# Kernel tuning notes

Measured on AMD Instinct MI355X. Metric: run time of the kernel, lower is better.

The kernel has to match this reference:

```python
import jax, jax.numpy as jnp
import numpy as np

TEMPERATURE = 0.1
EPS = 1e-12  # matches torch F.normalize eps


def setup_inputs() -> dict:
    key = jax.random.key(0)
    k1, k2 = jax.random.split(key)
    B, T, C = 8, 1024, 512
    x = jax.random.normal(k1, (B, T, C), dtype=jnp.float32)
    quantized = jax.random.normal(k2, (B, T, C), dtype=jnp.float32)
    return {"x": x, "quantized": quantized}


def reference(x, quantized):
    B, T, C = x.shape
    xf = x.reshape(-1, C)            # (N, C)
    qf = quantized.reshape(-1, C)    # (N, C)
    xn = xf / jnp.maximum(jnp.linalg.norm(xf, axis=-1, keepdims=True), EPS)
    qn = qf / jnp.maximum(jnp.linalg.norm(qf, axis=-1, keepdims=True), EPS)
    # (N, N) similarity logits
    sim = jnp.matmul(xn, qn.T) / TEMPERATURE
    N = sim.shape[0]
    # cross-entropy with targets = arange(N): loss_i = logsumexp(sim_i) - sim_ii
    logZ = jax.nn.logsumexp(sim, axis=-1)
    diag = jnp.diagonal(sim)
    loss = jnp.mean(logZ - diag)
    predictions = jnp.argmax(sim, axis=-1)
    targets = jnp.arange(N)
    accuracy = jnp.mean((predictions == targets).astype(jnp.float32))
    return loss, accuracy
```

## Files before the change

kernel.cpp:

```cpp
#include <hip/hip_runtime.h>
#include <hip/hip_bf16.h>
#include <math.h>

#define CDIM 512
#define NROW 8192
#define BM 256
#define BN 256
#define BK 32
#define NT 16
#define NCB 32
#define BUFSZ 32768
#define TEMP_INV 10.0f

typedef unsigned short u16;
typedef u16  u16x8 __attribute__((ext_vector_type(8)));
typedef __bf16 bf16x8 __attribute__((ext_vector_type(8)));
typedef float  f32x4 __attribute__((ext_vector_type(4)));

static __device__ __forceinline__ float bf2f(u16 u) {
    return __uint_as_float(((unsigned)u) << 16);
}
static __device__ __forceinline__ u16 f2bf(float f) {
    unsigned u = __float_as_uint(f);
    return (u16)((u + 0x7FFFu + ((u >> 16) & 1u)) >> 16);
}

static __device__ __forceinline__ void gload_lds16(const u16* g, char* l) {
    __builtin_amdgcn_global_load_lds(
        (const __attribute__((address_space(1))) void*)g,
        (__attribute__((address_space(3))) void*)l, 16, 0, 0);
}

__global__ __launch_bounds__(256) void norm_split_kernel(
    const float* __restrict__ x, const float* __restrict__ q,
    u16* __restrict__ xh, u16* __restrict__ qh, int n)
{
    int wave = blockIdx.x * 4 + (threadIdx.x >> 6);
    int lane = threadIdx.x & 63;
    const float* src; u16* dh; int row;
    if (wave < n) { src = x; dh = xh; row = wave; }
    else          { src = q; dh = qh; row = wave - n; }

    const float4* p = reinterpret_cast<const float4*>(src + (size_t)row * CDIM);
    float4 a = p[lane * 2];
    float4 b = p[lane * 2 + 1];
    float v[8] = {a.x, a.y, a.z, a.w, b.x, b.y, b.z, b.w};
    float ss = 0.f;
#pragma unroll
    for (int j = 0; j < 8; ++j) ss += v[j] * v[j];
#pragma unroll
    for (int off = 32; off; off >>= 1) ss += __shfl_xor(ss, off);
    float scale = 1.0f / fmaxf(sqrtf(ss), 1e-12f);

    u16 h[8] __attribute__((aligned(16)));
#pragma unroll
    for (int j = 0; j < 8; ++j) h[j] = f2bf(v[j] * scale);
    *(u16x8*)&dh[(size_t)row * CDIM + lane * 8] = *(u16x8*)h;
}

__global__ __launch_bounds__(1024, 4) void sim_main_kernel(
    const u16* __restrict__ xh, const u16* __restrict__ qh,
    float4* __restrict__ part)
{
    extern __shared__ __align__(16) char smem[];
    const int t = threadIdx.x, lane = t & 63, wid = t >> 6;
    const int wm = wid >> 2, wn = wid & 3;

    const int orig = blockIdx.x;
    const int xcd = orig & 7, s = orig >> 3;
    const int rb = s >> 2;
    const int cb = xcd * 4 + (s & 3);
    const int row0 = rb * BM, col0 = cb * BN;

    const int schunk = (t & 3) ^ ((t >> 3) & 3);
    const u16* sa = xh + (size_t)(row0 + (t >> 2)) * CDIM + schunk * 8;
    const u16* sb = qh + (size_t)(col0 + (t >> 2)) * CDIM + schunk * 8;
    const unsigned dstw = (unsigned)wid * 1024u;

    auto stage = [&](int kt) {
        char* b = smem + (kt % 3) * BUFSZ;
        const int ko = kt * BK;
        gload_lds16(sa + ko, b + dstw);
        gload_lds16(sb + ko, b + 16384 + dstw);
    };

    const unsigned kxc = ((unsigned)((lane >> 4) ^ ((lane >> 1) & 3))) * 16u;
    const unsigned aro = ((unsigned)(wm * 64 + (lane & 15))) * 64u + kxc;
    const unsigned bro = 16384u + ((unsigned)(wn * 64 + (lane & 15))) * 64u + kxc;

    f32x4 acc[4][4];
#pragma unroll
    for (int i = 0; i < 4; ++i)
#pragma unroll
        for (int j = 0; j < 4; ++j) acc[i][j] = (f32x4){0.f, 0.f, 0.f, 0.f};

    stage(0); stage(1);
    asm volatile("s_waitcnt vmcnt(2)" ::: "memory");
    __builtin_amdgcn_s_barrier();
    asm volatile("" ::: "memory");

    for (int kt = 0; kt < NT; ++kt) {
        const char* buf = smem + (kt % 3) * BUFSZ;
        if (kt < NT - 2) stage(kt + 2);
        bf16x8 afr[4], bfr[4];
#pragma unroll
        for (int mf = 0; mf < 4; ++mf) afr[mf] = *(const bf16x8*)(buf + aro + mf * 1024u);
#pragma unroll
        for (int nf = 0; nf < 4; ++nf) bfr[nf] = *(const bf16x8*)(buf + bro + nf * 1024u);

        __builtin_amdgcn_s_setprio(1);
#pragma unroll
        for (int mf = 0; mf < 4; ++mf)
#pragma unroll
            for (int nf = 0; nf < 4; ++nf)
                acc[mf][nf] = __builtin_amdgcn_mfma_f32_16x16x32_bf16(
                    afr[mf], bfr[nf], acc[mf][nf], 0, 0, 0);
        __builtin_amdgcn_s_setprio(0);

        if (kt < NT - 2)       { asm volatile("s_waitcnt vmcnt(2)" ::: "memory"); }
        else if (kt == NT - 2) { asm volatile("s_waitcnt vmcnt(0)" ::: "memory"); }
        asm volatile("s_waitcnt lgkmcnt(0)" ::: "memory");
        __builtin_amdgcn_s_barrier();
        asm volatile("" ::: "memory");
    }

    __syncthreads();
    float* sm = (float*)smem;
    float* sl = sm + 1024;
    int*   si = (int*)(sl + 1024);
    float* sd = (float*)(si + 1024);
    const int g = lane >> 4;
#pragma unroll
    for (int mf = 0; mf < 4; ++mf) {
#pragma unroll
        for (int r = 0; r < 4; ++r) {
            const int row_loc  = wm * 64 + mf * 16 + g * 4 + r;
            const int row_glob = row0 + row_loc;
            const int ci = col0 + wn * 64 + (lane & 15);
            float vmax = acc[mf][0][r];
            int cbest = ci;
#pragma unroll
            for (int nf = 1; nf < 4; ++nf) {
                float v = acc[mf][nf][r];
                if (v > vmax) { vmax = v; cbest = ci + nf * 16; }
                if (ci + nf * 16 == row_glob) sd[row_loc] = v * TEMP_INV;
            }
            if (ci == row_glob) sd[row_loc] = acc[mf][0][r] * TEMP_INV;
#pragma unroll
            for (int m = 1; m < 16; m <<= 1) {
                float ov = __shfl_xor(vmax, m);
                int   oi = __shfl_xor(cbest, m);
                if (ov > vmax || (ov == vmax && oi < cbest)) { vmax = ov; cbest = oi; }
            }
            float ssum = 0.f;
#pragma unroll
            for (int nf = 0; nf < 4; ++nf)
                ssum += __expf((acc[mf][nf][r] - vmax) * TEMP_INV);
#pragma unroll
            for (int m = 1; m < 16; m <<= 1) ssum += __shfl_xor(ssum, m);
            if ((lane & 15) == 0) {
                sm[row_loc * 4 + wn] = vmax * TEMP_INV;
                sl[row_loc * 4 + wn] = ssum;
                si[row_loc * 4 + wn] = cbest;
            }
        }
    }
    __syncthreads();
    if (t < 256) {
        float M = sm[t * 4];
#pragma unroll
        for (int w = 1; w < 4; ++w) M = fmaxf(M, sm[t * 4 + w]);
        float L = 0.f;
#pragma unroll
        for (int w = 0; w < 4; ++w) L += sl[t * 4 + w] * __expf(sm[t * 4 + w] - M);
        float bv = -1e30f; int bi = 0;
#pragma unroll
        for (int w = 0; w < 4; ++w) {
            float v = sm[t * 4 + w];
            if (v > bv) { bv = v; bi = si[t * 4 + w]; }
        }
        part[(size_t)(row0 + t) * NCB + cb] =
            make_float4(M, L, __int_as_float(bi), sd[t]);
    }
}

__global__ __launch_bounds__(256) void merge_kernel(
    const float4* __restrict__ part,
    float* __restrict__ loss_arr, float* __restrict__ corr_arr)
{
    int i    = blockIdx.x * 4 + (threadIdx.x >> 6);
    int lane = threadIdx.x & 63;
    float4 v = part[(size_t)i * NCB + (lane & 31)];

    float M = v.x;
#pragma unroll
    for (int off = 32; off; off >>= 1) M = fmaxf(M, __shfl_xor(M, off));
    float L = (lane < 32) ? v.y * __expf(v.x - M) : 0.f;
#pragma unroll
    for (int off = 32; off; off >>= 1) L += __shfl_xor(L, off);
    float bm = v.x; int bi = __float_as_int(v.z);
#pragma unroll
    for (int off = 1; off < 32; off <<= 1) {
        float ov = __shfl_xor(bm, off);
        int   oi = __shfl_xor(bi, off);
        if (ov > bm || (ov == bm && oi < bi)) { bm = ov; bi = oi; }
    }
    float dg = __shfl(v.w, i >> 8);
    if (lane == 0) {
        loss_arr[i] = (M + logf(L)) - dg;
        corr_arr[i] = (bi == i) ? 1.0f : 0.0f;
    }
}

__global__ __launch_bounds__(256) void finalize_kernel(
    const float* __restrict__ loss_arr, const float* __restrict__ corr_arr,
    float* __restrict__ out, int n)
{
    float a = 0.f, b = 0.f;
    for (int i = threadIdx.x; i < n; i += 256) { a += loss_arr[i]; b += corr_arr[i]; }
#pragma unroll
    for (int off = 32; off; off >>= 1) { a += __shfl_xor(a, off); b += __shfl_xor(b, off); }
    __shared__ float sa[4], sb[4];
    int wid = threadIdx.x >> 6, lane = threadIdx.x & 63;
    if (lane == 0) { sa[wid] = a; sb[wid] = b; }
    __syncthreads();
    if (threadIdx.x == 0) {
        out[0] = (sa[0] + sa[1] + sa[2] + sa[3]) / n;
        out[1] = (sb[0] + sb[1] + sb[2] + sb[3]) / n;
    }
}

extern "C" void kernel_launch(void* const* d_in, const int* in_sizes, int n_in,
                              void* d_out, int out_size, void* d_ws, size_t ws_size,
                              hipStream_t stream)
{
    const float* x = (const float*)d_in[0];
    const float* q = (const float*)d_in[1];
    const int n = in_sizes[0] / CDIM;

    char* ws = (char*)d_ws;
    size_t sz_bf = (size_t)n * CDIM * sizeof(u16);
    u16* xh = (u16*)(ws);
    u16* qh = (u16*)(ws + sz_bf);
    char* p = ws + 2 * sz_bf;
    float4* part = (float4*)p; p += (size_t)n * NCB * sizeof(float4);
    float* loss_arr = (float*)p; p += (size_t)n * 4;
    float* corr_arr = (float*)p;

    norm_split_kernel<<<(2 * n) / 4, 256, 0, stream>>>(x, q, xh, qh, n);

    sim_main_kernel<<<(n / BM) * (n / BN), 1024, 3 * BUFSZ, stream>>>(xh, qh, part);

    merge_kernel<<<n / 4, 256, 0, stream>>>(part, loss_arr, corr_arr);

    finalize_kernel<<<1, 256, 0, stream>>>(loss_arr, corr_arr, (float*)d_out, n);
}
```

Before: 122.6 us.

## Use 8-wave 128x64 warp tiles with BK=64 double-buffered phased pipeline

The similarity GEMM moves from 16 waves with 64x64 per-wave tiles, BK=32 and a triple buffer to 8 waves with 128x64 per-wave tiles, BK=64 and a 128KB double buffer. Each k-step is split into four phases, and each phase interleaves loading part of the next tile with MFMA work on the current one, using staged vmcnt waits and a new XOR swizzle. The aim is more register-level reuse per LDS read and fewer barriers per unit of work. The cost is fewer waves to hide latency, higher accumulator register pressure and a larger LDS footprint. The epilogue row mapping is updated to the new wave layout.

```diff
diff --git a/kernel.cpp b/kernel.cpp
--- a/kernel.cpp
+++ b/kernel.cpp
@@ -6,10 +6,9 @@
 #define NROW 8192
 #define BM 256
 #define BN 256
-#define BK 32
-#define NT 16
+#define BK 64
+#define NT 8
 #define NCB 32
-#define BUFSZ 32768
 #define TEMP_INV 10.0f
 
 typedef unsigned short u16;
@@ -58,7 +57,7 @@
     *(u16x8*)&dh[(size_t)row * CDIM + lane * 8] = *(u16x8*)h;
 }
 
-__global__ __launch_bounds__(1024, 4) void sim_main_kernel(
+__global__ __launch_bounds__(512, 2) void sim_main_kernel(
     const u16* __restrict__ xh, const u16* __restrict__ qh,
     float4* __restrict__ part)
 {
@@ -72,57 +71,103 @@
     const int cb = xcd * 4 + (s & 3);
     const int row0 = rb * BM, col0 = cb * BN;
 
-    const int schunk = (t & 3) ^ ((t >> 3) & 3);
-    const u16* sa = xh + (size_t)(row0 + (t >> 2)) * CDIM + schunk * 8;
-    const u16* sb = qh + (size_t)(col0 + (t >> 2)) * CDIM + schunk * 8;
-    const unsigned dstw = (unsigned)wid * 1024u;
-
-    auto stage = [&](int kt) {
-        char* b = smem + (kt % 3) * BUFSZ;
-        const int ko = kt * BK;
-        gload_lds16(sa + ko, b + dstw);
-        gload_lds16(sb + ko, b + 16384 + dstw);
-    };
-
-    const unsigned kxc = ((unsigned)((lane >> 4) ^ ((lane >> 1) & 3))) * 16u;
-    const unsigned aro = ((unsigned)(wm * 64 + (lane & 15))) * 64u + kxc;
-    const unsigned bro = 16384u + ((unsigned)(wn * 64 + (lane & 15))) * 64u + kxc;
-
-    f32x4 acc[4][4];
-#pragma unroll
-    for (int i = 0; i < 4; ++i)
+    const int hh = t >> 8;
+    const int rr = (t >> 3) & 31;
+    const int rB = t >> 3;
+    const unsigned blog = (((unsigned)t & 7u) * 16u) ^ ((((unsigned)t >> 3) & 7u) << 4);
+    const u16* sA = xh + (size_t)(row0 + hh * 128 + rr) * CDIM + blog / 2;
+    const u16* sB = qh + (size_t)(col0 + rB) * CDIM + blog / 2;
+
+    const unsigned kx0 = ((((unsigned)lane >> 4)) * 16u) ^ ((((unsigned)lane & 7u)) << 4);
+    const unsigned kx1 = (64u + (((unsigned)lane >> 4)) * 16u) ^ ((((unsigned)lane & 7u)) << 4);
+    const unsigned abase = (unsigned)wm * 4096u + (unsigned)(lane & 15) * 128u;
+    const unsigned bbase = 32768u + (unsigned)wn * 8192u + (unsigned)(lane & 15) * 128u;
+
+    f32x4 acc[8][4];
+#pragma unroll
+    for (int i = 0; i < 8; ++i)
 #pragma unroll
         for (int j = 0; j < 4; ++j) acc[i][j] = (f32x4){0.f, 0.f, 0.f, 0.f};
 
-    stage(0); stage(1);
-    asm volatile("s_waitcnt vmcnt(2)" ::: "memory");
+#define STAGE_A(BUF, KT, C) gload_lds16(sA + (size_t)(C) * (32 * CDIM) + (KT) * BK, \
+        smem + (BUF) * 65536 + (C) * 8192 + wid * 1024)
+#define STAGE_B(BUF, KT, W) gload_lds16(sB + (size_t)(W) * (64 * CDIM) + (KT) * BK, \
+        smem + (BUF) * 65536 + 32768 + (W) * 8192 + wid * 1024)
+
+#define READ_A(P)                                                              \
+    afr[0][0] = *(const bf16x8*)(buf + abase + (P) * 8192u + kx0);             \
+    afr[0][1] = *(const bf16x8*)(buf + abase + (P) * 8192u + kx1);             \
+    afr[1][0] = *(const bf16x8*)(buf + abase + (P) * 8192u + 2048u + kx0);     \
+    afr[1][1] = *(const bf16x8*)(buf + abase + (P) * 8192u + 2048u + kx1);
+
+#define PHASE_MFMA(MF0)                                                        \
+    __builtin_amdgcn_s_setprio(1);                                             \
+    _Pragma("unroll")                                                          \
+    for (int ks = 0; ks < 2; ++ks)                                             \
+        _Pragma("unroll")                                                      \
+        for (int m = 0; m < 2; ++m)                                            \
+            _Pragma("unroll")                                                  \
+            for (int nf = 0; nf < 4; ++nf)                                     \
+                acc[(MF0) + m][nf] = __builtin_amdgcn_mfma_f32_16x16x32_bf16(  \
+                    afr[m][ks], bfr[nf][ks], acc[(MF0) + m][nf], 0, 0, 0);     \
+    __builtin_amdgcn_s_setprio(0);
+
+#define BAR() asm volatile("" ::: "memory"); __builtin_amdgcn_s_barrier(); asm volatile("" ::: "memory")
+
+    STAGE_B(0, 0, 0); STAGE_B(0, 0, 1); STAGE_B(0, 0, 2); STAGE_B(0, 0, 3);
+    STAGE_A(0, 0, 0); STAGE_A(0, 0, 1); STAGE_A(0, 0, 2); STAGE_A(0, 0, 3);
+    asm volatile("s_waitcnt vmcnt(0)" ::: "memory");
     __builtin_amdgcn_s_barrier();
     asm volatile("" ::: "memory");
 
     for (int kt = 0; kt < NT; ++kt) {
-        const char* buf = smem + (kt % 3) * BUFSZ;
-        if (kt < NT - 2) stage(kt + 2);
-        bf16x8 afr[4], bfr[4];
-#pragma unroll
-        for (int mf = 0; mf < 4; ++mf) afr[mf] = *(const bf16x8*)(buf + aro + mf * 1024u);
-#pragma unroll
-        for (int nf = 0; nf < 4; ++nf) bfr[nf] = *(const bf16x8*)(buf + bro + nf * 1024u);
-
-        __builtin_amdgcn_s_setprio(1);
-#pragma unroll
-        for (int mf = 0; mf < 4; ++mf)
-#pragma unroll
-            for (int nf = 0; nf < 4; ++nf)
-                acc[mf][nf] = __builtin_amdgcn_mfma_f32_16x16x32_bf16(
-                    afr[mf], bfr[nf], acc[mf][nf], 0, 0, 0);
-        __builtin_amdgcn_s_setprio(0);
-
-        if (kt < NT - 2)       { asm volatile("s_waitcnt vmcnt(2)" ::: "memory"); }
-        else if (kt == NT - 2) { asm volatile("s_waitcnt vmcnt(0)" ::: "memory"); }
+        const char* buf = smem + (unsigned)(kt & 1) * 65536u;
+        const int nb = (kt + 1) & 1;
+        const bool pf = (kt + 1 < NT);
+        bf16x8 bfr[4][2], afr[2][2];
+
+        asm volatile("s_waitcnt vmcnt(3)" ::: "memory");
+#pragma unroll
+        for (int nf = 0; nf < 4; ++nf) {
+            bfr[nf][0] = *(const bf16x8*)(buf + bbase + nf * 2048u + kx0);
+            bfr[nf][1] = *(const bf16x8*)(buf + bbase + nf * 2048u + kx1);
+        }
+        READ_A(0)
+        if (pf) { STAGE_B(nb, kt + 1, 0); STAGE_B(nb, kt + 1, 1); }
+        BAR();
         asm volatile("s_waitcnt lgkmcnt(0)" ::: "memory");
-        __builtin_amdgcn_s_barrier();
-        asm volatile("" ::: "memory");
-    }
+        PHASE_MFMA(0)
+        BAR();
+
+        asm volatile("s_waitcnt vmcnt(4)" ::: "memory");
+        READ_A(1)
+        if (pf) { STAGE_B(nb, kt + 1, 2); STAGE_B(nb, kt + 1, 3); }
+        BAR();
+        asm volatile("s_waitcnt lgkmcnt(0)" ::: "memory");
+        PHASE_MFMA(2)
+        BAR();
+
+        asm volatile("s_waitcnt vmcnt(5)" ::: "memory");
+        READ_A(2)
+        if (pf) { STAGE_A(nb, kt + 1, 0); STAGE_A(nb, kt + 1, 1); }
+        BAR();
+        asm volatile("s_waitcnt lgkmcnt(0)" ::: "memory");
+        PHASE_MFMA(4)
+        BAR();
+
+        asm volatile("s_waitcnt vmcnt(6)" ::: "memory");
+        READ_A(3)
+        if (pf) { STAGE_A(nb, kt + 1, 2); STAGE_A(nb, kt + 1, 3); }
+        BAR();
+        asm volatile("s_waitcnt lgkmcnt(0)" ::: "memory");
+        PHASE_MFMA(6)
+        BAR();
+    }
+#undef STAGE_A
+#undef STAGE_B
+#undef READ_A
+#undef PHASE_MFMA
+#undef BAR
 
     __syncthreads();
     float* sm = (float*)smem;
@@ -131,10 +176,10 @@
     float* sd = (float*)(si + 1024);
     const int g = lane >> 4;
 #pragma unroll
-    for (int mf = 0; mf < 4; ++mf) {
+    for (int mf = 0; mf < 8; ++mf) {
 #pragma unroll
         for (int r = 0; r < 4; ++r) {
-            const int row_loc  = wm * 64 + mf * 16 + g * 4 + r;
+            const int row_loc  = wm * 128 + mf * 16 + g * 4 + r;
             const int row_glob = row0 + row_loc;
             const int ci = col0 + wn * 64 + (lane & 15);
             float vmax = acc[mf][0][r];
@@ -249,7 +294,7 @@
 
     norm_split_kernel<<<(2 * n) / 4, 256, 0, stream>>>(x, q, xh, qh, n);
 
-    sim_main_kernel<<<(n / BM) * (n / BN), 1024, 3 * BUFSZ, stream>>>(xh, qh, part);
+    sim_main_kernel<<<(n / BM) * (n / BN), 512, 131072, stream>>>(xh, qh, part);
 
     merge_kernel<<<n / 4, 256, 0, stream>>>(part, loss_arr, corr_arr);
 
```

Measured after the change: 156.3 us. 1.27x slower.

## Persistent blocks loop over column tiles, stream B from global, fixed-shift logsumexp

Applied to the files above, without the earlier changes.

The sim kernel now launches 256 blocks of 512 threads. Each block owns a 256-row A tile and loops over four column tiles. A is staged in LDS through a triple buffer, while each warp loads its B fragments straight from global into registers, double-buffered across k-steps, and computes a 128x64 sub-tile. The logsumexp drops the running max and subtracts a fixed constant of 10, which relies on unit-normalized vectors bounding logits by 1/T, so the merge skips its max rescale. This cuts LDS traffic and launch count, but it lowers occupancy, raises register pressure, and makes B reads uncoalesced per lane.

```diff
diff --git a/kernel.cpp b/kernel.cpp
--- a/kernel.cpp
+++ b/kernel.cpp
@@ -7,9 +7,8 @@
 #define BM 256
 #define BN 256
 #define BK 32
-#define NT 16
+#define GTOT 64
 #define NCB 32
-#define BUFSZ 32768
 #define TEMP_INV 10.0f
 
 typedef unsigned short u16;
@@ -58,130 +57,152 @@
     *(u16x8*)&dh[(size_t)row * CDIM + lane * 8] = *(u16x8*)h;
 }
 
-__global__ __launch_bounds__(1024, 4) void sim_main_kernel(
+__global__ __launch_bounds__(512, 2) void sim_main_kernel(
     const u16* __restrict__ xh, const u16* __restrict__ qh,
     float4* __restrict__ part)
 {
     extern __shared__ __align__(16) char smem[];
     const int t = threadIdx.x, lane = t & 63, wid = t >> 6;
     const int wm = wid >> 2, wn = wid & 3;
-
-    const int orig = blockIdx.x;
-    const int xcd = orig & 7, s = orig >> 3;
-    const int rb = s >> 2;
-    const int cb = xcd * 4 + (s & 3);
-    const int row0 = rb * BM, col0 = cb * BN;
+    const int xcd = blockIdx.x & 7, rb = blockIdx.x >> 3;
+    const int row0 = rb * BM;
 
     const int schunk = (t & 3) ^ ((t >> 3) & 3);
-    const u16* sa = xh + (size_t)(row0 + (t >> 2)) * CDIM + schunk * 8;
-    const u16* sb = qh + (size_t)(col0 + (t >> 2)) * CDIM + schunk * 8;
-    const unsigned dstw = (unsigned)wid * 1024u;
-
-    auto stage = [&](int kt) {
-        char* b = smem + (kt % 3) * BUFSZ;
-        const int ko = kt * BK;
-        gload_lds16(sa + ko, b + dstw);
-        gload_lds16(sb + ko, b + 16384 + dstw);
-    };
+    const u16* sa0 = xh + (size_t)(row0 + (t >> 2)) * CDIM + schunk * 8;
+    const u16* sa1 = sa0 + 128 * CDIM;
 
     const unsigned kxc = ((unsigned)((lane >> 4) ^ ((lane >> 1) & 3))) * 16u;
-    const unsigned aro = ((unsigned)(wm * 64 + (lane & 15))) * 64u + kxc;
-    const unsigned bro = 16384u + ((unsigned)(wn * 64 + (lane & 15))) * 64u + kxc;
-
-    f32x4 acc[4][4];
-#pragma unroll
-    for (int i = 0; i < 4; ++i)
-#pragma unroll
-        for (int j = 0; j < 4; ++j) acc[i][j] = (f32x4){0.f, 0.f, 0.f, 0.f};
-
-    stage(0); stage(1);
-    asm volatile("s_waitcnt vmcnt(2)" ::: "memory");
+    const unsigned aro = ((unsigned)(wm * 128 + (lane & 15))) * 64u + kxc;
+
+    const u16* pBl = qh + (size_t)(lane & 15) * CDIM + (lane >> 4) * 8;
+
+#define STAGE_A(G) do {                                                        \
+        char* b_ = smem + ((G) % 3) * 16384;                                   \
+        const int ko_ = ((G) & 15) * BK;                                       \
+        gload_lds16(sa0 + ko_, b_ + wid * 1024);                               \
+        gload_lds16(sa1 + ko_, b_ + 8192 + wid * 1024);                        \
+    } while (0)
+
+#define LOAD_B(DST, GN) do {                                                   \
+        const int col0n_ = (xcd * 4 + ((GN) >> 4)) * BN;                       \
+        const u16* pn_ = pBl + (size_t)(col0n_ + wn * 64) * CDIM               \
+                         + ((GN) & 15) * BK;                                   \
+        _Pragma("unroll")                                                      \
+        for (int nf_ = 0; nf_ < 4; ++nf_)                                      \
+            DST[nf_] = *(const bf16x8*)(pn_ + (size_t)nf_ * 16 * CDIM);        \
+    } while (0)
+
+    f32x4 acc[8][4];
+    bf16x8 Bc[4], Bn[4];
+
+    STAGE_A(0); STAGE_A(1);
+    LOAD_B(Bc, 0);
+    asm volatile("s_waitcnt vmcnt(6)" ::: "memory");
     __builtin_amdgcn_s_barrier();
     asm volatile("" ::: "memory");
 
-    for (int kt = 0; kt < NT; ++kt) {
-        const char* buf = smem + (kt % 3) * BUFSZ;
-        if (kt < NT - 2) stage(kt + 2);
-        bf16x8 afr[4], bfr[4];
-#pragma unroll
-        for (int mf = 0; mf < 4; ++mf) afr[mf] = *(const bf16x8*)(buf + aro + mf * 1024u);
-#pragma unroll
-        for (int nf = 0; nf < 4; ++nf) bfr[nf] = *(const bf16x8*)(buf + bro + nf * 1024u);
-
-        __builtin_amdgcn_s_setprio(1);
-#pragma unroll
-        for (int mf = 0; mf < 4; ++mf)
-#pragma unroll
-            for (int nf = 0; nf < 4; ++nf)
-                acc[mf][nf] = __builtin_amdgcn_mfma_f32_16x16x32_bf16(
-                    afr[mf], bfr[nf], acc[mf][nf], 0, 0, 0);
-        __builtin_amdgcn_s_setprio(0);
-
-        if (kt < NT - 2)       { asm volatile("s_waitcnt vmcnt(2)" ::: "memory"); }
-        else if (kt == NT - 2) { asm volatile("s_waitcnt vmcnt(0)" ::: "memory"); }
-        asm volatile("s_waitcnt lgkmcnt(0)" ::: "memory");
-        __builtin_amdgcn_s_barrier();
-        asm volatile("" ::: "memory");
-    }
-
-    __syncthreads();
-    float* sm = (float*)smem;
-    float* sl = sm + 1024;
-    int*   si = (int*)(sl + 1024);
-    float* sd = (float*)(si + 1024);
-    const int g = lane >> 4;
-#pragma unroll
-    for (int mf = 0; mf < 4; ++mf) {
-#pragma unroll
-        for (int r = 0; r < 4; ++r) {
-            const int row_loc  = wm * 64 + mf * 16 + g * 4 + r;
-            const int row_glob = row0 + row_loc;
-            const int ci = col0 + wn * 64 + (lane & 15);
-            float vmax = acc[mf][0][r];
-            int cbest = ci;
-#pragma unroll
-            for (int nf = 1; nf < 4; ++nf) {
-                float v = acc[mf][nf][r];
-                if (v > vmax) { vmax = v; cbest = ci + nf * 16; }
-                if (ci + nf * 16 == row_glob) sd[row_loc] = v * TEMP_INV;
-            }
-            if (ci == row_glob) sd[row_loc] = acc[mf][0][r] * TEMP_INV;
-#pragma unroll
-            for (int m = 1; m < 16; m <<= 1) {
-                float ov = __shfl_xor(vmax, m);
-                int   oi = __shfl_xor(cbest, m);
-                if (ov > vmax || (ov == vmax && oi < cbest)) { vmax = ov; cbest = oi; }
-            }
-            float ssum = 0.f;
-#pragma unroll
-            for (int nf = 0; nf < 4; ++nf)
-                ssum += __expf((acc[mf][nf][r] - vmax) * TEMP_INV);
-#pragma unroll
-            for (int m = 1; m < 16; m <<= 1) ssum += __shfl_xor(ssum, m);
-            if ((lane & 15) == 0) {
-                sm[row_loc * 4 + wn] = vmax * TEMP_INV;
-                sl[row_loc * 4 + wn] = ssum;
-                si[row_loc * 4 + wn] = cbest;
+#define KT_HALF(KT, CUR, NXT)                                                  \
+    {                                                                          \
+        const int g = c * 16 + (KT);                                           \
+        if ((KT) < 14 || c < 3) STAGE_A(g + 2);                                \
+        if ((KT) < 15 || c < 3) LOAD_B(NXT, g + 1);                            \
+        const char* buf = smem + (g % 3) * 16384;                              \
+        bf16x8 afr[8];                                                         \
+        _Pragma("unroll")                                                      \
+        for (int mf = 0; mf < 8; ++mf)                                         \
+            afr[mf] = *(const bf16x8*)(buf + aro + mf * 1024u);                \
+        if ((KT) == 15 && c == 3) { asm volatile("s_waitcnt vmcnt(0)" ::: "memory"); } \
+        else                      { asm volatile("s_waitcnt vmcnt(6)" ::: "memory"); } \
+        __builtin_amdgcn_s_setprio(1);                                         \
+        _Pragma("unroll")                                                      \
+        for (int mf = 0; mf < 8; ++mf)                                         \
+            _Pragma("unroll")                                                  \
+            for (int nf = 0; nf < 4; ++nf)                                     \
+                acc[mf][nf] = __builtin_amdgcn_mfma_f32_16x16x32_bf16(         \
+                    afr[mf], CUR[nf], acc[mf][nf], 0, 0, 0);                   \
+        __builtin_amdgcn_s_setprio(0);                                         \
+        asm volatile("s_waitcnt lgkmcnt(0)" ::: "memory");                     \
+        __builtin_amdgcn_s_barrier();                                          \
+        asm volatile("" ::: "memory");                                         \
+    }
+
+    for (int c = 0; c < 4; ++c) {
+        const int cb = xcd * 4 + c;
+        const int col0 = cb * BN;
+
+#pragma unroll
+        for (int i = 0; i < 8; ++i)
+#pragma unroll
+            for (int j = 0; j < 4; ++j) acc[i][j] = (f32x4){0.f, 0.f, 0.f, 0.f};
+
+#pragma unroll
+        for (int kt2 = 0; kt2 < 8; ++kt2) {
+            KT_HALF(kt2 * 2,     Bc, Bn)
+            KT_HALF(kt2 * 2 + 1, Bn, Bc)
+        }
+
+        __syncthreads();
+        float* sm = (float*)(smem + 49152);
+        float* sl = sm + 1024;
+        int*   si = (int*)(sl + 1024);
+        float* sd = (float*)(si + 1024);
+        const int g4 = lane >> 4;
+#pragma unroll
+        for (int mf = 0; mf < 8; ++mf) {
+#pragma unroll
+            for (int r = 0; r < 4; ++r) {
+                const int row_loc  = wm * 128 + mf * 16 + g4 * 4 + r;
+                const int row_glob = row0 + row_loc;
+                const int ci = col0 + wn * 64 + (lane & 15);
+                float vmax = acc[mf][0][r];
+                int cbest = ci;
+#pragma unroll
+                for (int nf = 1; nf < 4; ++nf) {
+                    float v = acc[mf][nf][r];
+                    if (v > vmax) { vmax = v; cbest = ci + nf * 16; }
+                    if (ci + nf * 16 == row_glob) sd[row_loc] = v * TEMP_INV;
+                }
+                if (ci == row_glob) sd[row_loc] = acc[mf][0][r] * TEMP_INV;
+#pragma unroll
+                for (int m = 1; m < 16; m <<= 1) {
+                    float ov = __shfl_xor(vmax, m);
+                    int   oi = __shfl_xor(cbest, m);
+                    if (ov > vmax || (ov == vmax && oi < cbest)) { vmax = ov; cbest = oi; }
+                }
+                float ssum = 0.f;
+#pragma unroll
+                for (int nf = 0; nf < 4; ++nf)
+                    ssum += __expf(acc[mf][nf][r] * TEMP_INV - 10.0f);
+#pragma unroll
+                for (int m = 1; m < 16; m <<= 1) ssum += __shfl_xor(ssum, m);
+                if ((lane & 15) == 0) {
+                    sm[row_loc * 4 + wn] = vmax * TEMP_INV;
+                    sl[row_loc * 4 + wn] = ssum;
+                    si[row_loc * 4 + wn] = cbest;
+                }
             }
         }
-    }
-    __syncthreads();
-    if (t < 256) {
-        float M = sm[t * 4];
-#pragma unroll
-        for (int w = 1; w < 4; ++w) M = fmaxf(M, sm[t * 4 + w]);
-        float L = 0.f;
-#pragma unroll
-        for (int w = 0; w < 4; ++w) L += sl[t * 4 + w] * __expf(sm[t * 4 + w] - M);
-        float bv = -1e30f; int bi = 0;
-#pragma unroll
-        for (int w = 0; w < 4; ++w) {
-            float v = sm[t * 4 + w];
-            if (v > bv) { bv = v; bi = si[t * 4 + w]; }
+        __syncthreads();
+        if (t < 256) {
+            float M = sm[t * 4];
+#pragma unroll
+            for (int w = 1; w < 4; ++w) M = fmaxf(M, sm[t * 4 + w]);
+            float L = 0.f;
+#pragma unroll
+            for (int w = 0; w < 4; ++w) L += sl[t * 4 + w];
+            float bv = -1e30f; int bi = 0;
+#pragma unroll
+            for (int w = 0; w < 4; ++w) {
+                float v = sm[t * 4 + w];
+                if (v > bv) { bv = v; bi = si[t * 4 + w]; }
+            }
+            part[(size_t)(row0 + t) * NCB + cb] =
+                make_float4(M, L, __int_as_float(bi), sd[t]);
         }
-        part[(size_t)(row0 + t) * NCB + cb] =
-            make_float4(M, L, __int_as_float(bi), sd[t]);
-    }
+    }
+#undef KT_HALF
+#undef STAGE_A
+#undef LOAD_B
 }
 
 __global__ __launch_bounds__(256) void merge_kernel(
@@ -192,10 +213,7 @@
     int lane = threadIdx.x & 63;
     float4 v = part[(size_t)i * NCB + (lane & 31)];
 
-    float M = v.x;
-#pragma unroll
-    for (int off = 32; off; off >>= 1) M = fmaxf(M, __shfl_xor(M, off));
-    float L = (lane < 32) ? v.y * __expf(v.x - M) : 0.f;
+    float L = (lane < 32) ? v.y : 0.f;
 #pragma unroll
     for (int off = 32; off; off >>= 1) L += __shfl_xor(L, off);
     float bm = v.x; int bi = __float_as_int(v.z);
@@ -207,7 +225,7 @@
     }
     float dg = __shfl(v.w, i >> 8);
     if (lane == 0) {
-        loss_arr[i] = (M + logf(L)) - dg;
+        loss_arr[i] = (10.0f + logf(L)) - dg;
         corr_arr[i] = (bi == i) ? 1.0f : 0.0f;
     }
 }
@@ -249,7 +267,7 @@
 
     norm_split_kernel<<<(2 * n) / 4, 256, 0, stream>>>(x, q, xh, qh, n);
 
-    sim_main_kernel<<<(n / BM) * (n / BN), 1024, 3 * BUFSZ, stream>>>(xh, qh, part);
+    sim_main_kernel<<<256, 512, 62464, stream>>>(xh, qh, part);
 
     merge_kernel<<<n / 4, 256, 0, stream>>>(part, loss_arr, corr_arr);
 
```

Result: slower. 276.2 us (+125.3%).

## Double-buffer LDS fragments in registers to overlap reads with MFMA

Applied to the files above, without the earlier changes.

Restructures the K loop so the LDS fragments for the next k-tile are loaded into a second register set while the MFMAs for the current tile run. The global-to-LDS stage issue, the wait and the barrier move to the top of each step, and the loop is fully unrolled with ping-pong fragment arrays. The aim is to hide LDS read latency behind matrix math instead of stalling before each MFMA block. In exchange it uses more VGPRs for fragments and produces larger unrolled code, which could lower occupancy.

```diff
diff --git a/kernel.cpp b/kernel.cpp
--- a/kernel.cpp
+++ b/kernel.cpp
@@ -94,35 +94,57 @@
 #pragma unroll
         for (int j = 0; j < 4; ++j) acc[i][j] = (f32x4){0.f, 0.f, 0.f, 0.f};
 
+    bf16x8 af0[4], bf0[4], af1[4], bf1[4];
+
     stage(0); stage(1);
     asm volatile("s_waitcnt vmcnt(2)" ::: "memory");
     __builtin_amdgcn_s_barrier();
     asm volatile("" ::: "memory");
-
-    for (int kt = 0; kt < NT; ++kt) {
-        const char* buf = smem + (kt % 3) * BUFSZ;
-        if (kt < NT - 2) stage(kt + 2);
-        bf16x8 afr[4], bfr[4];
-#pragma unroll
-        for (int mf = 0; mf < 4; ++mf) afr[mf] = *(const bf16x8*)(buf + aro + mf * 1024u);
-#pragma unroll
-        for (int nf = 0; nf < 4; ++nf) bfr[nf] = *(const bf16x8*)(buf + bro + nf * 1024u);
-
-        __builtin_amdgcn_s_setprio(1);
-#pragma unroll
-        for (int mf = 0; mf < 4; ++mf)
-#pragma unroll
-            for (int nf = 0; nf < 4; ++nf)
-                acc[mf][nf] = __builtin_amdgcn_mfma_f32_16x16x32_bf16(
-                    afr[mf], bfr[nf], acc[mf][nf], 0, 0, 0);
-        __builtin_amdgcn_s_setprio(0);
-
-        if (kt < NT - 2)       { asm volatile("s_waitcnt vmcnt(2)" ::: "memory"); }
-        else if (kt == NT - 2) { asm volatile("s_waitcnt vmcnt(0)" ::: "memory"); }
-        asm volatile("s_waitcnt lgkmcnt(0)" ::: "memory");
-        __builtin_amdgcn_s_barrier();
-        asm volatile("" ::: "memory");
-    }
+    {
+        const char* buf = smem;
+#pragma unroll
+        for (int mf = 0; mf < 4; ++mf) af0[mf] = *(const bf16x8*)(buf + aro + mf * 1024u);
+#pragma unroll
+        for (int nf = 0; nf < 4; ++nf) bf0[nf] = *(const bf16x8*)(buf + bro + nf * 1024u);
+    }
+
+#define KT_STEP(KT, CA, CB, NA, NB)                                            \
+    {                                                                          \
+        if ((KT) < NT - 2) {                                                   \
+            stage((KT) + 2);                                                   \
+            asm volatile("s_waitcnt vmcnt(2)" ::: "memory");                   \
+        } else if ((KT) == NT - 2) {                                           \
+            asm volatile("s_waitcnt vmcnt(0)" ::: "memory");                   \
+        }                                                                      \
+        asm volatile("s_waitcnt lgkmcnt(0)" ::: "memory");                     \
+        __builtin_amdgcn_s_barrier();                                          \
+        asm volatile("" ::: "memory");                                         \
+        if ((KT) < NT - 1) {                                                   \
+            const char* nbuf = smem + (((KT) + 1) % 3) * BUFSZ;                \
+            _Pragma("unroll")                                                  \
+            for (int mf = 0; mf < 4; ++mf)                                     \
+                NA[mf] = *(const bf16x8*)(nbuf + aro + mf * 1024u);            \
+            _Pragma("unroll")                                                  \
+            for (int nf = 0; nf < 4; ++nf)                                     \
+                NB[nf] = *(const bf16x8*)(nbuf + bro + nf * 1024u);            \
+        }                                                                      \
+        asm volatile("" ::: "memory");                                         \
+        __builtin_amdgcn_s_setprio(1);                                         \
+        _Pragma("unroll")                                                      \
+        for (int mf = 0; mf < 4; ++mf)                                         \
+            _Pragma("unroll")                                                  \
+            for (int nf = 0; nf < 4; ++nf)                                     \
+                acc[mf][nf] = __builtin_amdgcn_mfma_f32_16x16x32_bf16(         \
+                    CA[mf], CB[nf], acc[mf][nf], 0, 0, 0);                     \
+        __builtin_amdgcn_s_setprio(0);                                         \
+    }
+
+#pragma unroll
+    for (int kt2 = 0; kt2 < 8; ++kt2) {
+        KT_STEP(kt2 * 2,     af0, bf0, af1, bf1)
+        KT_STEP(kt2 * 2 + 1, af1, bf1, af0, bf0)
+    }
+#undef KT_STEP
 
     __syncthreads();
     float* sm = (float*)smem;
```

New measurement: 250.5 us. 2.04x slower.
